# Kernel optimization log

Hardware: AMD Instinct MI355X
Metric: run time of the kernel (lower is better)

The kernel has to match this reference:

```python
import jax, jax.numpy as jnp
import numpy as np

PATCH = 16  # patch_size: unfold kernel == stride


def setup_inputs() -> dict:
    key = jax.random.key(0)
    k1, k2 = jax.random.split(key)
    x = jax.random.normal(k1, (32, 128, 128, 128), dtype=jnp.float32)          # [b, n, h, w]
    conv_w = jax.random.normal(k2, (128, 128, 3, 3), dtype=jnp.float32) * 0.02  # [out_c, in_c, kh, kw]
    return {"x": x, "conv_w": conv_w}


def reference(x, conv_w):
    b, n, h, w = x.shape
    p = PATCH
    nh, nw = h // p, w // p
    bn = b * n
    P = nh * nw  # number of patches per (b, n) slice

    # unfold(1, p, p).unfold(2, p, p): [bn, nh, nw, p, p]
    a = x.reshape(bn, nh, p, nw, p).transpose(0, 1, 3, 2, 4).reshape(bn, P, p, p)
    a1 = a.reshape(bn, P, p * p)

    # patch-to-patch affinity + softmax: [bn, P, P]
    f1 = jnp.einsum('bie,bje->bij', a1, a1)
    f_div_C = jax.nn.softmax(f1, axis=-1)

    # AdaptiveAvgPool2d(1) over each patch -> per-patch mean: [bn, P]
    y1 = a.mean(axis=(-2, -1))

    # attention-weighted patch means: [bn, P] -> [b, n, nh, nw]
    y2 = jnp.einsum('bij,bj->bi', f_div_C, y1).reshape(b, n, nh, nw)

    # 3x3 conv, stride 1, SAME padding, no bias
    y2 = jax.lax.conv_general_dilated(
        y2, conv_w, window_strides=(1, 1), padding='SAME',
        dimension_numbers=('NCHW', 'OIHW', 'NCHW'))

    # global average pool -> [b, n, 1, 1]
    return y2.mean(axis=(2, 3), keepdims=True)
```

## Files before the change

kernel.cpp:

```cpp
#include <hip/hip_runtime.h>


typedef __attribute__((ext_vector_type(8))) short short8;
typedef __attribute__((ext_vector_type(4))) float f32x4;

#define RS 264

__device__ __forceinline__ ushort f2bf(float f) {
    unsigned u = __float_as_uint(f);
    u += 0x7FFF + ((u >> 16) & 1);
    return (ushort)(u >> 16);
}

__global__ __launch_bounds__(256, 4)
void k1_attn(const float* __restrict__ x, float* __restrict__ y2g) {
    __shared__ __align__(16) ushort A[64 * RS];
    __shared__ float y1sc[64 * 9];
    __shared__ float y1f[64];

    const int slice = blockIdx.x;
    const int tid   = threadIdx.x;
    const int lane  = tid & 63;
    const int w     = tid >> 6;

    const float4* xs4 = (const float4*)(x + (size_t)slice * 16384);
    float4 st[16];
#pragma unroll
    for (int it = 0; it < 16; ++it) st[it] = xs4[it * 256 + tid];

    const int pc = (tid & 31) >> 2;
    const int s  = tid >> 5;
    const int c4 = tid & 3;

#pragma unroll
    for (int pb = 0; pb < 8; ++pb) {
        const float4 v0 = st[2 * pb], v1 = st[2 * pb + 1];
        float part = (v0.x + v0.y + v0.z + v0.w) + (v1.x + v1.y + v1.z + v1.w);
        part += __shfl_xor(part, 1);
        part += __shfl_xor(part, 2);
        if (c4 == 0) y1sc[(tid >> 2) * 9 + pb] = part;
        const int p = pb * 8 + pc;
        ushort4 b0 = make_ushort4(f2bf(v0.x), f2bf(v0.y), f2bf(v0.z), f2bf(v0.w));
        ushort4 b1 = make_ushort4(f2bf(v1.x), f2bf(v1.y), f2bf(v1.z), f2bf(v1.w));
        *(ushort4*)&A[p * RS + s * 16 + c4 * 4]       = b0;
        *(ushort4*)&A[p * RS + (8 + s) * 16 + c4 * 4] = b1;
    }
    __syncthreads();

    if (tid < 64) {
        const int opb = tid >> 3, opc = tid & 7;
        float sum = 0.f;
#pragma unroll
        for (int a = 0; a < 8; ++a) sum += y1sc[(a * 8 + opc) * 9 + opb];
        y1f[tid] = sum * (1.f / 256.f);
    }
    __syncthreads();

    const int l15 = lane & 15, lg = lane >> 4;
    const int r0  = w * 16;

    float y1c[4];
#pragma unroll
    for (int c = 0; c < 4; ++c) y1c[c] = y1f[c * 16 + l15];

    f32x4 acc[4];
#pragma unroll
    for (int c = 0; c < 4; ++c) acc[c] = (f32x4){0.f, 0.f, 0.f, 0.f};

#pragma unroll
    for (int kk = 0; kk < 8; ++kk) {
        const int ko = kk * 32 + lg * 8;
        short8 af = *(const short8*)&A[(r0 + l15) * RS + ko];
#pragma unroll
        for (int c = 0; c < 4; ++c) {
            short8 bf = *(const short8*)&A[(c * 16 + l15) * RS + ko];
            acc[c] = __builtin_amdgcn_mfma_f32_16x16x32_bf16(af, bf, acc[c], 0, 0, 0);
        }
    }

#pragma unroll
    for (int r = 0; r < 4; ++r) {
        const float v0 = acc[0][r], v1 = acc[1][r], v2 = acc[2][r], v3 = acc[3][r];
        float mx = fmaxf(fmaxf(v0, v1), fmaxf(v2, v3));
        mx = fmaxf(mx, __shfl_xor(mx, 1));
        mx = fmaxf(mx, __shfl_xor(mx, 2));
        mx = fmaxf(mx, __shfl_xor(mx, 4));
        mx = fmaxf(mx, __shfl_xor(mx, 8));
        const float e0 = __expf(v0 - mx), e1 = __expf(v1 - mx);
        const float e2 = __expf(v2 - mx), e3 = __expf(v3 - mx);
        float sum = e0 + e1 + e2 + e3;
        float num = e0 * y1c[0] + e1 * y1c[1] + e2 * y1c[2] + e3 * y1c[3];
        sum += __shfl_xor(sum, 1); num += __shfl_xor(num, 1);
        sum += __shfl_xor(sum, 2); num += __shfl_xor(num, 2);
        sum += __shfl_xor(sum, 4); num += __shfl_xor(num, 4);
        sum += __shfl_xor(sum, 8); num += __shfl_xor(num, 8);
        if (l15 == 0) y2g[(size_t)slice * 64 + r0 + lg * 4 + r] = num / sum;
    }
}

__global__ __launch_bounds__(128, 4)
void k2_conv(const float* __restrict__ y2g, const float* __restrict__ cw,
             float* __restrict__ out) {
    __shared__ __align__(16) float y2s[128 * 68];
    __shared__ __align__(16) float Tf[1152];
    const int b = blockIdx.x;
    const int t = threadIdx.x;

    const float4* src = (const float4*)(y2g + (size_t)b * 8192);
#pragma unroll
    for (int it = 0; it < 16; ++it) {
        const int fi = it * 128 + t;
        float4 v = src[fi];
        *(float4*)&y2s[(fi >> 4) * 68 + (fi & 15) * 4] = v;
    }
    __syncthreads();

    {
        float g[64];
#pragma unroll
        for (int q = 0; q < 16; ++q) {
            float4 v = *(const float4*)&y2s[t * 68 + q * 4];
            g[4 * q + 0] = v.x; g[4 * q + 1] = v.y; g[4 * q + 2] = v.z; g[4 * q + 3] = v.w;
        }
        float R[8], C[8], S = 0.f;
#pragma unroll
        for (int r = 0; r < 8; ++r) { R[r] = 0.f; C[r] = 0.f; }
#pragma unroll
        for (int r = 0; r < 8; ++r)
#pragma unroll
            for (int c = 0; c < 8; ++c) { R[r] += g[8 * r + c]; C[c] += g[8 * r + c]; }
#pragma unroll
        for (int r = 0; r < 8; ++r) S += R[r];
#pragma unroll
        for (int kh = 0; kh < 3; ++kh)
#pragma unroll
            for (int kw = 0; kw < 3; ++kw) {
                float v = S;
                if (kh == 0) v -= R[7]; else if (kh == 2) v -= R[0];
                if (kw == 0) v -= C[7]; else if (kw == 2) v -= C[0];
                if (kh != 1 && kw != 1) {
                    const int er = (kh == 0) ? 7 : 0;
                    const int ec = (kw == 0) ? 7 : 0;
                    v += g[8 * er + ec];
                }
                Tf[t * 9 + kh * 3 + kw] = v;
            }
    }
    __syncthreads();

    {
        const int wv = t >> 6, ln = t & 63, gg = ln >> 4, j16 = ln & 15;
#pragma unroll 2
        for (int pass = 0; pass < 16; ++pass) {
            const int oc = pass * 8 + wv * 4 + gg;
            const float4* wp = (const float4*)(cw + (size_t)oc * 1152);
            float acc = 0.f;
#pragma unroll
            for (int it = 0; it < 18; ++it) {
                const float4 a  = wp[it * 16 + j16];
                const float4 tt = *(const float4*)&Tf[(it * 16 + j16) * 4];
                acc += a.x * tt.x + a.y * tt.y + a.z * tt.z + a.w * tt.w;
            }
            acc += __shfl_xor(acc, 1);
            acc += __shfl_xor(acc, 2);
            acc += __shfl_xor(acc, 4);
            acc += __shfl_xor(acc, 8);
            if (j16 == 0) out[b * 128 + oc] = acc * (1.f / 64.f);
        }
    }
}

extern "C" void kernel_launch(void* const* d_in, const int* in_sizes, int n_in,
                              void* d_out, int out_size, void* d_ws, size_t ws_size,
                              hipStream_t stream) {
    const float* x  = (const float*)d_in[0];
    const float* cw = (const float*)d_in[1];
    float* out = (float*)d_out;
    float* y2g = (float*)d_ws;

    hipLaunchKernelGGL(k1_attn, dim3(4096), dim3(256), 0, stream, x, y2g);
    hipLaunchKernelGGL(k2_conv, dim3(32), dim3(128), 0, stream, y2g, cw, out);
}
```

Before: 375.1 us.

## Compute patch means via MFMA with ones and split conv across more blocks

```diff
diff --git a/kernel.cpp b/kernel.cpp
--- a/kernel.cpp
+++ b/kernel.cpp
@@ -1,4 +1,5 @@
 #include <hip/hip_runtime.h>
+#include <hip/hip_bf16.h>
 
 
 typedef __attribute__((ext_vector_type(8))) short short8;
@@ -7,16 +8,12 @@
 #define RS 264
 
 __device__ __forceinline__ ushort f2bf(float f) {
-    unsigned u = __float_as_uint(f);
-    u += 0x7FFF + ((u >> 16) & 1);
-    return (ushort)(u >> 16);
+    return __bfloat16_as_ushort(__float2bfloat16(f));
 }
 
 __global__ __launch_bounds__(256, 4)
 void k1_attn(const float* __restrict__ x, float* __restrict__ y2g) {
     __shared__ __align__(16) ushort A[64 * RS];
-    __shared__ float y1sc[64 * 9];
-    __shared__ float y1f[64];
 
     const int slice = blockIdx.x;
     const int tid   = threadIdx.x;
@@ -35,10 +32,6 @@
 #pragma unroll
     for (int pb = 0; pb < 8; ++pb) {
         const float4 v0 = st[2 * pb], v1 = st[2 * pb + 1];
-        float part = (v0.x + v0.y + v0.z + v0.w) + (v1.x + v1.y + v1.z + v1.w);
-        part += __shfl_xor(part, 1);
-        part += __shfl_xor(part, 2);
-        if (c4 == 0) y1sc[(tid >> 2) * 9 + pb] = part;
         const int p = pb * 8 + pc;
         ushort4 b0 = make_ushort4(f2bf(v0.x), f2bf(v0.y), f2bf(v0.z), f2bf(v0.w));
         ushort4 b1 = make_ushort4(f2bf(v1.x), f2bf(v1.y), f2bf(v1.z), f2bf(v1.w));
@@ -47,25 +40,16 @@
     }
     __syncthreads();
 
-    if (tid < 64) {
-        const int opb = tid >> 3, opc = tid & 7;
-        float sum = 0.f;
-#pragma unroll
-        for (int a = 0; a < 8; ++a) sum += y1sc[(a * 8 + opc) * 9 + opb];
-        y1f[tid] = sum * (1.f / 256.f);
-    }
-    __syncthreads();
-
     const int l15 = lane & 15, lg = lane >> 4;
     const int r0  = w * 16;
 
-    float y1c[4];
+    f32x4 acc[4], accY[4];
 #pragma unroll
-    for (int c = 0; c < 4; ++c) y1c[c] = y1f[c * 16 + l15];
+    for (int c = 0; c < 4; ++c) { acc[c] = (f32x4){0,0,0,0}; accY[c] = (f32x4){0,0,0,0}; }
 
-    f32x4 acc[4];
+    short8 ones;
 #pragma unroll
-    for (int c = 0; c < 4; ++c) acc[c] = (f32x4){0.f, 0.f, 0.f, 0.f};
+    for (int q = 0; q < 8; ++q) ones[q] = (short)0x3F80;
 
 #pragma unroll
     for (int kk = 0; kk < 8; ++kk) {
@@ -74,9 +58,14 @@
 #pragma unroll
         for (int c = 0; c < 4; ++c) {
             short8 bf = *(const short8*)&A[(c * 16 + l15) * RS + ko];
-            acc[c] = __builtin_amdgcn_mfma_f32_16x16x32_bf16(af, bf, acc[c], 0, 0, 0);
+            acc[c]  = __builtin_amdgcn_mfma_f32_16x16x32_bf16(af,   bf, acc[c],  0, 0, 0);
+            accY[c] = __builtin_amdgcn_mfma_f32_16x16x32_bf16(ones, bf, accY[c], 0, 0, 0);
         }
     }
+
+    float y1c[4];
+#pragma unroll
+    for (int c = 0; c < 4; ++c) y1c[c] = accY[c][0] * (1.f / 256.f);
 
 #pragma unroll
     for (int r = 0; r < 4; ++r) {
@@ -101,9 +90,9 @@
 __global__ __launch_bounds__(128, 4)
 void k2_conv(const float* __restrict__ y2g, const float* __restrict__ cw,
              float* __restrict__ out) {
-    __shared__ __align__(16) float y2s[128 * 68];
+    __shared__ __align__(16) float y2s[128 * 72];
     __shared__ __align__(16) float Tf[1152];
-    const int b = blockIdx.x;
+    const int b = blockIdx.x >> 2, q = blockIdx.x & 3;
     const int t = threadIdx.x;
 
     const float4* src = (const float4*)(y2g + (size_t)b * 8192);
@@ -111,16 +100,16 @@
     for (int it = 0; it < 16; ++it) {
         const int fi = it * 128 + t;
         float4 v = src[fi];
-        *(float4*)&y2s[(fi >> 4) * 68 + (fi & 15) * 4] = v;
+        *(float4*)&y2s[(fi >> 4) * 72 + (fi & 15) * 4] = v;
     }
     __syncthreads();
 
     {
         float g[64];
 #pragma unroll
-        for (int q = 0; q < 16; ++q) {
-            float4 v = *(const float4*)&y2s[t * 68 + q * 4];
-            g[4 * q + 0] = v.x; g[4 * q + 1] = v.y; g[4 * q + 2] = v.z; g[4 * q + 3] = v.w;
+        for (int qq = 0; qq < 16; ++qq) {
+            float4 v = *(const float4*)&y2s[t * 72 + qq * 4];
+            g[4 * qq + 0] = v.x; g[4 * qq + 1] = v.y; g[4 * qq + 2] = v.z; g[4 * qq + 3] = v.w;
         }
         float R[8], C[8], S = 0.f;
 #pragma unroll
@@ -150,9 +139,9 @@
 
     {
         const int wv = t >> 6, ln = t & 63, gg = ln >> 4, j16 = ln & 15;
-#pragma unroll 2
-        for (int pass = 0; pass < 16; ++pass) {
-            const int oc = pass * 8 + wv * 4 + gg;
+#pragma unroll
+        for (int pass = 0; pass < 4; ++pass) {
+            const int oc = q * 32 + pass * 8 + wv * 4 + gg;
             const float4* wp = (const float4*)(cw + (size_t)oc * 1152);
             float acc = 0.f;
 #pragma unroll
@@ -179,5 +168,5 @@
     float* y2g = (float*)d_ws;
 
     hipLaunchKernelGGL(k1_attn, dim3(4096), dim3(256), 0, stream, x, y2g);
-    hipLaunchKernelGGL(k2_conv, dim3(32), dim3(128), 0, stream, y2g, cw, out);
+    hipLaunchKernelGGL(k2_conv, dim3(128), dim3(128), 0, stream, y2g, cw, out);
 }
```

Measured after the change: 364.6 us. -2.8%, faster.
